# Optimization experiments

Measured on AMD Instinct MI355X. Metric: run time of the kernel, lower is better.

Reference implementation:

```python
import jax, jax.numpy as jnp
import numpy as np

IN = 1    # input feature dim (hardcoded in NN)
H = 10    # LSTM hidden size (hardcoded in NN)
B = 8192  # batch
T = 256   # sequence length


def setup_inputs() -> dict:
    key = jax.random.key(0)
    ks = jax.random.split(key, 12)
    s = 0.1  # init scale for mus (mimics blitz posterior_mu_init spread)
    RHO0 = -3.0  # posterior_rho_init from the module
    return {
        "x": jax.random.normal(ks[0], (B, T, IN), jnp.float32),
        # BayesianLSTM variational parameters (blitz layout: (in, 4*H), (H, 4*H), (4*H,))
        "w_ih_mu": jax.random.normal(ks[1], (IN, 4 * H), jnp.float32) * s,
        "w_ih_rho": jnp.full((IN, 4 * H), RHO0, jnp.float32),
        "w_hh_mu": jax.random.normal(ks[2], (H, 4 * H), jnp.float32) * s,
        "w_hh_rho": jnp.full((H, 4 * H), RHO0, jnp.float32),
        "b_mu": jax.random.normal(ks[3], (4 * H,), jnp.float32) * s,
        "b_rho": jnp.full((4 * H,), RHO0, jnp.float32),
        # reparameterization noise, sampled once per forward call in blitz
        "eps_ih": jax.random.normal(ks[4], (IN, 4 * H), jnp.float32),
        "eps_hh": jax.random.normal(ks[5], (H, 4 * H), jnp.float32),
        "eps_b": jax.random.normal(ks[6], (4 * H,), jnp.float32),
        # deterministic linear head nn.Linear(10, 1)
        "lin_w": jax.random.normal(ks[7], (1, H), jnp.float32) * s,
        "lin_b": jnp.zeros((1,), jnp.float32),
    }


def reference(x, w_ih_mu, w_ih_rho, w_hh_mu, w_hh_rho, b_mu, b_rho,
              eps_ih, eps_hh, eps_b, lin_w, lin_b):
    sp = jax.nn.softplus
    # sample weights: w = mu + log1p(exp(rho)) * eps
    w_ih = w_ih_mu + sp(w_ih_rho) * eps_ih   # (IN, 4H)
    w_hh = w_hh_mu + sp(w_hh_rho) * eps_hh   # (H, 4H)
    b = b_mu + sp(b_rho) * eps_b             # (4H,)

    # precompute input contribution for all timesteps: (B, T, 4H)
    x_proj = jnp.einsum('bti,ig->btg', x, w_ih) + b

    def step(carry, xg):
        h, c = carry                      # (B, H) each
        gates = xg + h @ w_hh             # (B, 4H)
        i = jax.nn.sigmoid(gates[:, :H])
        f = jax.nn.sigmoid(gates[:, H:2 * H])
        g = jnp.tanh(gates[:, 2 * H:3 * H])
        o = jax.nn.sigmoid(gates[:, 3 * H:])
        c = f * c + i * g
        h = o * jnp.tanh(c)
        return (h, c), None

    h0 = jnp.zeros((x.shape[0], H), x.dtype)
    (h_last, _), _ = jax.lax.scan(step, (h0, h0), jnp.swapaxes(x_proj, 0, 1))
    # NN takes hidden_seq[:, -1, :] == final hidden state, then linear head
    return h_last @ lin_w.T + lin_b  # (B, 1)
```

## Files before the change

### kernel.cpp

```cpp
#include <hip/hip_runtime.h>
#include <math.h>

#define T_LEN 256
#define HID 10

template <int PAT>
__device__ __forceinline__ float swz(float v) {
    return __int_as_float(__builtin_amdgcn_ds_swizzle(__float_as_int(v), PAT));
}

__device__ __forceinline__ float softplus_f(float x) {
    return fmaxf(x, 0.0f) + log1pf(expf(-fabsf(x)));
}
__device__ __forceinline__ float samp(const float* mu, const float* rho,
                                      const float* eps, int i) {
    return mu[i] + softplus_f(rho[i]) * eps[i];
}

__device__ __forceinline__ float fast_sigmoid(float x) {
    float e = __builtin_amdgcn_exp2f(-1.442695040888963f * x);
    return __builtin_amdgcn_rcpf(1.0f + e);
}
__device__ __forceinline__ float fast_tanh(float x) {
    float e = __builtin_amdgcn_exp2f(2.885390081777927f * x);
    return fmaf(-2.0f, __builtin_amdgcn_rcpf(e + 1.0f), 1.0f);
}

#define GATES(HV, XT, CC, HK)                                            \
    {                                                                    \
        float gi = fmaf((XT), wih[0], bs[0]);                            \
        float gf = fmaf((XT), wih[1], bs[1]);                            \
        float gg = fmaf((XT), wih[2], bs[2]);                            \
        float go = fmaf((XT), wih[3], bs[3]);                            \
        _Pragma("unroll")                                                \
        for (int j = 0; j < HID; ++j) {                                  \
            gi = fmaf(HV[j], whi[j], gi);                                \
            gf = fmaf(HV[j], whf[j], gf);                                \
            gg = fmaf(HV[j], whg[j], gg);                                \
            go = fmaf(HV[j], who[j], go);                                \
        }                                                                \
        float si = fast_sigmoid(gi);                                     \
        float sf = fast_sigmoid(gf);                                     \
        float tg = fast_tanh(gg);                                        \
        float so = fast_sigmoid(go);                                     \
        (CC) = fmaf(sf, (CC), si * tg);                                  \
        (HK) = so * fast_tanh(CC);                                       \
    }

#define TSTEP(TI)                                                        \
    {                                                                    \
        float4 hA0 = *(const float4*)(hbA);                              \
        float4 hA1 = *(const float4*)(hbA + 4);                          \
        float2 hA2 = *(const float2*)(hbA + 8);                          \
        float4 hB0 = *(const float4*)(hbB);                              \
        float4 hB1 = *(const float4*)(hbB + 4);                          \
        float2 hB2 = *(const float2*)(hbB + 8);                          \
        float xa = swz<((TI) << 5) | 0x10>(xcA);                         \
        float xb = swz<((TI) << 5) | 0x10>(xcB);                         \
        float hvA[HID] = {hA0.x, hA0.y, hA0.z, hA0.w,                    \
                          hA1.x, hA1.y, hA1.z, hA1.w, hA2.x, hA2.y};     \
        float hvB[HID] = {hB0.x, hB0.y, hB0.z, hB0.w,                    \
                          hB1.x, hB1.y, hB1.z, hB1.w, hB2.x, hB2.y};     \
        GATES(hvA, xa, cA, hkA);                                         \
        GATES(hvB, xb, cB, hkB);                                         \
        wrA[0] = hkA;                                                    \
        wrB[0] = hkB;                                                    \
    }

__global__ __launch_bounds__(256) void bayes_lstm_kernel(
    const float* __restrict__ x,
    const float* __restrict__ w_ih_mu, const float* __restrict__ w_ih_rho,
    const float* __restrict__ w_hh_mu, const float* __restrict__ w_hh_rho,
    const float* __restrict__ b_mu,    const float* __restrict__ b_rho,
    const float* __restrict__ eps_ih,  const float* __restrict__ eps_hh,
    const float* __restrict__ eps_b,
    const float* __restrict__ lin_w,   const float* __restrict__ lin_b,
    float* __restrict__ out)
{
    __shared__ __align__(16) float hbuf[16 * 2 * 20];

    const int tid  = threadIdx.x;
    const int k    = tid & 15;
    const int slot = tid >> 4;
    const int bA   = (blockIdx.x * 16 + slot) * 2;
    const int bB   = bA + 1;

    float* hbA = hbuf + (slot * 2 + 0) * 20;
    float* hbB = hbuf + (slot * 2 + 1) * 20;
    float* wrA = hbA + k;
    float* wrB = hbB + k;

    float whi[HID], whf[HID], whg[HID], who[HID];
    float wih[4] = {0.f, 0.f, 0.f, 0.f};
    float bs[4]  = {0.f, 0.f, 0.f, 0.f};
    float lw = 0.f;
#pragma unroll
    for (int j = 0; j < HID; ++j) { whi[j] = 0.f; whf[j] = 0.f; whg[j] = 0.f; who[j] = 0.f; }

    if (k < HID) {
        const int c0 = k, c1 = HID + k, c2 = 2 * HID + k, c3 = 3 * HID + k;
        wih[0] = samp(w_ih_mu, w_ih_rho, eps_ih, c0);
        wih[1] = samp(w_ih_mu, w_ih_rho, eps_ih, c1);
        wih[2] = samp(w_ih_mu, w_ih_rho, eps_ih, c2);
        wih[3] = samp(w_ih_mu, w_ih_rho, eps_ih, c3);
        bs[0]  = samp(b_mu, b_rho, eps_b, c0);
        bs[1]  = samp(b_mu, b_rho, eps_b, c1);
        bs[2]  = samp(b_mu, b_rho, eps_b, c2);
        bs[3]  = samp(b_mu, b_rho, eps_b, c3);
#pragma unroll
        for (int j = 0; j < HID; ++j) {
            whi[j] = samp(w_hh_mu, w_hh_rho, eps_hh, j * 4 * HID + c0);
            whf[j] = samp(w_hh_mu, w_hh_rho, eps_hh, j * 4 * HID + c1);
            whg[j] = samp(w_hh_mu, w_hh_rho, eps_hh, j * 4 * HID + c2);
            who[j] = samp(w_hh_mu, w_hh_rho, eps_hh, j * 4 * HID + c3);
        }
        lw = lin_w[k];
    }

    wrA[0] = 0.f;
    wrB[0] = 0.f;

    float cA = 0.f, cB = 0.f, hkA = 0.f, hkB = 0.f;
    const float* xrA = x + (size_t)bA * T_LEN;
    const float* xrB = x + (size_t)bB * T_LEN;
    float xcA = xrA[k];
    float xcB = xrB[k];

    for (int to = 0; to < 16; ++to) {
        float xnA = 0.f, xnB = 0.f;
        if (to < 15) {
            xnA = xrA[(to + 1) * 16 + k];
            xnB = xrB[(to + 1) * 16 + k];
        }
        TSTEP(0)  TSTEP(1)  TSTEP(2)  TSTEP(3)
        TSTEP(4)  TSTEP(5)  TSTEP(6)  TSTEP(7)
        TSTEP(8)  TSTEP(9)  TSTEP(10) TSTEP(11)
        TSTEP(12) TSTEP(13) TSTEP(14) TSTEP(15)
        xcA = xnA; xcB = xnB;
    }

    float pa = hkA * lw;
    float pb = hkB * lw;
    pa += __shfl_xor(pa, 1, 16);  pb += __shfl_xor(pb, 1, 16);
    pa += __shfl_xor(pa, 2, 16);  pb += __shfl_xor(pb, 2, 16);
    pa += __shfl_xor(pa, 4, 16);  pb += __shfl_xor(pb, 4, 16);
    pa += __shfl_xor(pa, 8, 16);  pb += __shfl_xor(pb, 8, 16);
    if (k == 0) {
        float b0 = lin_b[0];
        out[bA] = pa + b0;
        out[bB] = pb + b0;
    }
}

extern "C" void kernel_launch(void* const* d_in, const int* in_sizes, int n_in,
                              void* d_out, int out_size, void* d_ws, size_t ws_size,
                              hipStream_t stream) {
    const float* x        = (const float*)d_in[0];
    const float* w_ih_mu  = (const float*)d_in[1];
    const float* w_ih_rho = (const float*)d_in[2];
    const float* w_hh_mu  = (const float*)d_in[3];
    const float* w_hh_rho = (const float*)d_in[4];
    const float* b_mu     = (const float*)d_in[5];
    const float* b_rho    = (const float*)d_in[6];
    const float* eps_ih   = (const float*)d_in[7];
    const float* eps_hh   = (const float*)d_in[8];
    const float* eps_b    = (const float*)d_in[9];
    const float* lin_w    = (const float*)d_in[10];
    const float* lin_b    = (const float*)d_in[11];
    float* out = (float*)d_out;

    const int n_b = in_sizes[0] / T_LEN;
    dim3 grid(n_b / 32), block(256);
    hipLaunchKernelGGL(bayes_lstm_kernel, grid, block, 0, stream,
                       x, w_ih_mu, w_ih_rho, w_hh_mu, w_hh_rho, b_mu, b_rho,
                       eps_ih, eps_hh, eps_b, lin_w, lin_b, out);
}
```

Before: 177.2 us.

## Pack gate FMAs into v2f, prefetch h after write, stream x via scalar loads

```diff
diff --git a/kernel.cpp b/kernel.cpp
--- a/kernel.cpp
+++ b/kernel.cpp
@@ -3,6 +3,8 @@
 
 #define T_LEN 256
 #define HID 10
+
+typedef float v2f __attribute__((ext_vector_type(2)));
 
 template <int PAT>
 __device__ __forceinline__ float swz(float v) {
@@ -26,45 +28,30 @@
     return fmaf(-2.0f, __builtin_amdgcn_rcpf(e + 1.0f), 1.0f);
 }
 
-#define GATES(HV, XT, CC, HK)                                            \
-    {                                                                    \
-        float gi = fmaf((XT), wih[0], bs[0]);                            \
-        float gf = fmaf((XT), wih[1], bs[1]);                            \
-        float gg = fmaf((XT), wih[2], bs[2]);                            \
-        float go = fmaf((XT), wih[3], bs[3]);                            \
-        _Pragma("unroll")                                                \
-        for (int j = 0; j < HID; ++j) {                                  \
-            gi = fmaf(HV[j], whi[j], gi);                                \
-            gf = fmaf(HV[j], whf[j], gf);                                \
-            gg = fmaf(HV[j], whg[j], gg);                                \
-            go = fmaf(HV[j], who[j], go);                                \
-        }                                                                \
-        float si = fast_sigmoid(gi);                                     \
-        float sf = fast_sigmoid(gf);                                     \
-        float tg = fast_tanh(gg);                                        \
-        float so = fast_sigmoid(go);                                     \
-        (CC) = fmaf(sf, (CC), si * tg);                                  \
-        (HK) = so * fast_tanh(CC);                                       \
-    }
+#define DOTJ(J, HV)                                                    \
+    hh.x = hh.y = (HV);                                                \
+    a01 = __builtin_elementwise_fma(hh, whh01[J], a01);                \
+    a23 = __builtin_elementwise_fma(hh, whh23[J], a23);
 
-#define TSTEP(TI)                                                        \
-    {                                                                    \
-        float4 hA0 = *(const float4*)(hbA);                              \
-        float4 hA1 = *(const float4*)(hbA + 4);                          \
-        float2 hA2 = *(const float2*)(hbA + 8);                          \
-        float4 hB0 = *(const float4*)(hbB);                              \
-        float4 hB1 = *(const float4*)(hbB + 4);                          \
-        float2 hB2 = *(const float2*)(hbB + 8);                          \
-        float xa = swz<((TI) << 5) | 0x10>(xcA);                         \
-        float xb = swz<((TI) << 5) | 0x10>(xcB);                         \
-        float hvA[HID] = {hA0.x, hA0.y, hA0.z, hA0.w,                    \
-                          hA1.x, hA1.y, hA1.z, hA1.w, hA2.x, hA2.y};     \
-        float hvB[HID] = {hB0.x, hB0.y, hB0.z, hB0.w,                    \
-                          hB1.x, hB1.y, hB1.z, hB1.w, hB2.x, hB2.y};     \
-        GATES(hvA, xa, cA, hkA);                                         \
-        GATES(hvB, xb, cB, hkB);                                         \
-        wrA[0] = hkA;                                                    \
-        wrB[0] = hkB;                                                    \
+#define ELEM_STEP(H0, H1, H2, XV, CC, HK, HB, WR)                      \
+    {                                                                  \
+        v2f hh;                                                        \
+        hh.x = hh.y = (XV);                                            \
+        v2f a01 = __builtin_elementwise_fma(hh, wih01, bb01);          \
+        v2f a23 = __builtin_elementwise_fma(hh, wih23, bb23);          \
+        DOTJ(0, (H0).x) DOTJ(1, (H0).y) DOTJ(2, (H0).z) DOTJ(3, (H0).w)\
+        DOTJ(4, (H1).x) DOTJ(5, (H1).y) DOTJ(6, (H1).z) DOTJ(7, (H1).w)\
+        DOTJ(8, (H2).x) DOTJ(9, (H2).y)                                \
+        float si = fast_sigmoid(a01.x);                                \
+        float sf = fast_sigmoid(a01.y);                                \
+        float tg = fast_tanh(a23.x);                                   \
+        float so = fast_sigmoid(a23.y);                                \
+        (CC) = fmaf(sf, (CC), si * tg);                                \
+        (HK) = so * fast_tanh(CC);                                     \
+        (WR)[0] = (HK);                                                \
+        (H0) = *(const float4*)(HB);                                   \
+        (H1) = *(const float4*)((HB) + 4);                             \
+        (H2) = *(const float2*)((HB) + 8);                             \
     }
 
 __global__ __launch_bounds__(256) void bayes_lstm_kernel(
@@ -90,61 +77,62 @@
     float* wrA = hbA + k;
     float* wrB = hbB + k;
 
-    float whi[HID], whf[HID], whg[HID], who[HID];
-    float wih[4] = {0.f, 0.f, 0.f, 0.f};
-    float bs[4]  = {0.f, 0.f, 0.f, 0.f};
+    v2f whh01[HID], whh23[HID];
+    v2f wih01, wih23, bb01, bb23;
+    wih01.x = wih01.y = 0.f; wih23.x = wih23.y = 0.f;
+    bb01.x = bb01.y = 0.f;   bb23.x = bb23.y = 0.f;
     float lw = 0.f;
 #pragma unroll
-    for (int j = 0; j < HID; ++j) { whi[j] = 0.f; whf[j] = 0.f; whg[j] = 0.f; who[j] = 0.f; }
-
+    for (int j = 0; j < HID; ++j) {
+        whh01[j].x = whh01[j].y = 0.f;
+        whh23[j].x = whh23[j].y = 0.f;
+    }
     if (k < HID) {
         const int c0 = k, c1 = HID + k, c2 = 2 * HID + k, c3 = 3 * HID + k;
-        wih[0] = samp(w_ih_mu, w_ih_rho, eps_ih, c0);
-        wih[1] = samp(w_ih_mu, w_ih_rho, eps_ih, c1);
-        wih[2] = samp(w_ih_mu, w_ih_rho, eps_ih, c2);
-        wih[3] = samp(w_ih_mu, w_ih_rho, eps_ih, c3);
-        bs[0]  = samp(b_mu, b_rho, eps_b, c0);
-        bs[1]  = samp(b_mu, b_rho, eps_b, c1);
-        bs[2]  = samp(b_mu, b_rho, eps_b, c2);
-        bs[3]  = samp(b_mu, b_rho, eps_b, c3);
+        wih01.x = samp(w_ih_mu, w_ih_rho, eps_ih, c0);
+        wih01.y = samp(w_ih_mu, w_ih_rho, eps_ih, c1);
+        wih23.x = samp(w_ih_mu, w_ih_rho, eps_ih, c2);
+        wih23.y = samp(w_ih_mu, w_ih_rho, eps_ih, c3);
+        bb01.x  = samp(b_mu, b_rho, eps_b, c0);
+        bb01.y  = samp(b_mu, b_rho, eps_b, c1);
+        bb23.x  = samp(b_mu, b_rho, eps_b, c2);
+        bb23.y  = samp(b_mu, b_rho, eps_b, c3);
 #pragma unroll
         for (int j = 0; j < HID; ++j) {
-            whi[j] = samp(w_hh_mu, w_hh_rho, eps_hh, j * 4 * HID + c0);
-            whf[j] = samp(w_hh_mu, w_hh_rho, eps_hh, j * 4 * HID + c1);
-            whg[j] = samp(w_hh_mu, w_hh_rho, eps_hh, j * 4 * HID + c2);
-            who[j] = samp(w_hh_mu, w_hh_rho, eps_hh, j * 4 * HID + c3);
+            whh01[j].x = samp(w_hh_mu, w_hh_rho, eps_hh, j * 4 * HID + c0);
+            whh01[j].y = samp(w_hh_mu, w_hh_rho, eps_hh, j * 4 * HID + c1);
+            whh23[j].x = samp(w_hh_mu, w_hh_rho, eps_hh, j * 4 * HID + c2);
+            whh23[j].y = samp(w_hh_mu, w_hh_rho, eps_hh, j * 4 * HID + c3);
         }
         lw = lin_w[k];
     }
 
-    wrA[0] = 0.f;
-    wrB[0] = 0.f;
+    float4 hA0 = {0,0,0,0}, hA1 = {0,0,0,0};
+    float4 hB0 = {0,0,0,0}, hB1 = {0,0,0,0};
+    float2 hA2v = {0,0}, hB2v = {0,0};
+    float cA = 0.f, cB = 0.f, hkA = 0.f, hkB = 0.f;
 
-    float cA = 0.f, cB = 0.f, hkA = 0.f, hkB = 0.f;
     const float* xrA = x + (size_t)bA * T_LEN;
     const float* xrB = x + (size_t)bB * T_LEN;
-    float xcA = xrA[k];
-    float xcB = xrB[k];
+    float xA0 = xrA[0], xA1 = xrA[1];
+    float xB0 = xrB[0], xB1 = xrB[1];
 
-    for (int to = 0; to < 16; ++to) {
-        float xnA = 0.f, xnB = 0.f;
-        if (to < 15) {
-            xnA = xrA[(to + 1) * 16 + k];
-            xnB = xrB[(to + 1) * 16 + k];
-        }
-        TSTEP(0)  TSTEP(1)  TSTEP(2)  TSTEP(3)
-        TSTEP(4)  TSTEP(5)  TSTEP(6)  TSTEP(7)
-        TSTEP(8)  TSTEP(9)  TSTEP(10) TSTEP(11)
-        TSTEP(12) TSTEP(13) TSTEP(14) TSTEP(15)
-        xcA = xnA; xcB = xnB;
+#pragma unroll 16
+    for (int t = 0; t < T_LEN; ++t) {
+        float xA2 = xrA[(t + 2) & (T_LEN - 1)];
+        float xB2 = xrB[(t + 2) & (T_LEN - 1)];
+        ELEM_STEP(hA0, hA1, hA2v, xA0, cA, hkA, hbA, wrA)
+        ELEM_STEP(hB0, hB1, hB2v, xB0, cB, hkB, hbB, wrB)
+        xA0 = xA1; xA1 = xA2;
+        xB0 = xB1; xB1 = xB2;
     }
 
     float pa = hkA * lw;
     float pb = hkB * lw;
-    pa += __shfl_xor(pa, 1, 16);  pb += __shfl_xor(pb, 1, 16);
-    pa += __shfl_xor(pa, 2, 16);  pb += __shfl_xor(pb, 2, 16);
-    pa += __shfl_xor(pa, 4, 16);  pb += __shfl_xor(pb, 4, 16);
-    pa += __shfl_xor(pa, 8, 16);  pb += __shfl_xor(pb, 8, 16);
+    pa += swz<(1 << 10) | 0x1f>(pa);  pb += swz<(1 << 10) | 0x1f>(pb);
+    pa += swz<(2 << 10) | 0x1f>(pa);  pb += swz<(2 << 10) | 0x1f>(pb);
+    pa += swz<(4 << 10) | 0x1f>(pa);  pb += swz<(4 << 10) | 0x1f>(pb);
+    pa += swz<(8 << 10) | 0x1f>(pa);  pb += swz<(8 << 10) | 0x1f>(pb);
     if (k == 0) {
         float b0 = lin_b[0];
         out[bA] = pa + b0;
```

Measured after the change: 177.4 us. Within noise of the previous version (+0.1%).
